# Performance work log

Measured on AMD Instinct MI355X. Metric: run time of the kernel, lower is better.

Reference implementation:

```python
import jax, jax.numpy as jnp
import numpy as np

B, T, DIM, S, DFF = 4, 2048, 2048, 4, 8192
SINKHORN_ITERS = 10


def setup_inputs() -> dict:
    key = jax.random.key(0)
    ks = jax.random.split(key, 12)

    def lin(k, fan_in, shape):
        bound = 1.0 / np.sqrt(fan_in)
        return jax.random.uniform(k, shape, jnp.float32, -bound, bound)

    return {
        "x": jax.random.normal(ks[0], (B, T, DIM), jnp.float32),
        # phi_* linears act on the S-times tiled vector of size S*DIM
        "phi_pre_w": lin(ks[1], S * DIM, (S, S * DIM)),
        "phi_pre_b": lin(ks[2], S * DIM, (S,)),
        "phi_post_w": lin(ks[3], S * DIM, (S, S * DIM)),
        "phi_post_b": lin(ks[4], S * DIM, (S,)),
        "phi_res_w": lin(ks[5], S * DIM, (S * S, S * DIM)),
        "phi_res_b": lin(ks[6], S * DIM, (S * S,)),
        "alpha_pre": jnp.ones((1,), jnp.float32),
        "alpha_post": jnp.ones((1,), jnp.float32),
        "alpha_res": jnp.ones((1,), jnp.float32),
        "b_pre": jnp.zeros((S,), jnp.float32),
        "b_post": jnp.zeros((S,), jnp.float32),
        "b_res": jnp.zeros((S, S), jnp.float32),
        # block = transformer MLP
        "W1": lin(ks[7], DIM, (DIM, DFF)),
        "b1": lin(ks[8], DIM, (DFF,)),
        "W2": lin(ks[9], DFF, (DFF, DIM)),
        "b2": lin(ks[10], DFF, (DIM,)),
    }


def sinkhorn_knopp(logits):
    # logits: [B, T, S, S] -> doubly-stochastic via exp + alternating normalization
    M = jnp.exp(logits)
    for _ in range(SINKHORN_ITERS):
        M = M / jnp.sum(M, axis=-1, keepdims=True)  # rows
        M = M / jnp.sum(M, axis=-2, keepdims=True)  # cols
    return M


def reference(x, phi_pre_w, phi_pre_b, phi_post_w, phi_post_b, phi_res_w,
              phi_res_b, alpha_pre, alpha_post, alpha_res, b_pre, b_post,
              b_res, W1, b1, W2, b2):
    bs, seq, d = x.shape
    s = b_pre.shape[0]
    eps = jnp.asarray(jnp.finfo(x.dtype).eps, x.dtype)
    # x_l = x expanded over S identical streams; x_vec = tile(x, S).
    # RMS over the tiled S*d vector == RMS over d (streams are copies).
    x_n = x * jax.lax.rsqrt(jnp.mean(x * x, axis=-1, keepdims=True) + eps)
    # Linear on the tiled vector == sum of the S weight blocks applied to x_n.
    Wp = phi_pre_w.reshape(s, s, d).sum(axis=1)        # [S, d]
    Wq = phi_post_w.reshape(s, s, d).sum(axis=1)       # [S, d]
    Wr = phi_res_w.reshape(s * s, s, d).sum(axis=1)    # [S*S, d]
    h_pre_t = alpha_pre * (jnp.einsum('btd,sd->bts', x_n, Wp) + phi_pre_b) + b_pre
    h_post_t = alpha_post * (jnp.einsum('btd,sd->bts', x_n, Wq) + phi_post_b) + b_post
    h_res_t = alpha_res * (jnp.einsum('btd,kd->btk', x_n, Wr) + phi_res_b)
    h_res_t = h_res_t.reshape(bs, seq, s, s) + b_res
    h_pre = jax.nn.sigmoid(h_pre_t)                    # [B,T,S]
    h_post = 2.0 * jax.nn.sigmoid(h_post_t)            # [B,T,S]
    h_res = sinkhorn_knopp(h_res_t)                    # [B,T,S,S]
    # block_input = sum_j x_l[:,:,j] * h_pre[...,j] ; streams identical -> x * sum_j h_pre
    block_input = x * jnp.sum(h_pre, axis=-1, keepdims=True)
    # block: MLP with exact (erf) GELU, matching torch default
    h = jax.nn.gelu(jnp.einsum('btd,df->btf', block_input, W1) + b1, approximate=False)
    block_out = jnp.einsum('btf,fd->btd', h, W2) + b2
    # out = sum_i [ (h_res @ x_l)_i + h_post_i * block_out ]
    #     = x * sum_{ij} h_res[ij] + block_out * sum_i h_post_i
    res_mix = jnp.sum(h_res, axis=(-2, -1))[..., None]         # [B,T,1]
    post_mix = jnp.sum(h_post, axis=-1, keepdims=True)          # [B,T,1]
    return x * res_mix + block_out * post_mix
```

## Files before the change

kernel.cpp:

```cpp
#include <hip/hip_runtime.h>
#include <hip/hip_bf16.h>
#include <cstdint>
#include <cstddef>

#define DIM   2048
#define DFF   8192
#define NROWS 8192
#define NFOLD 24

typedef float f32x4 __attribute__((ext_vector_type(4)));
typedef __bf16 bf16x8 __attribute__((ext_vector_type(8)));

__device__ __forceinline__ float sigmoidf_(float v) { return 1.0f / (1.0f + expf(-v)); }

__device__ __forceinline__ unsigned short f2bf(float v) {
    union { __hip_bfloat16 h; unsigned short u; } cv;
    cv.h = __float2bfloat16(v);
    return cv.u;
}

__device__ __forceinline__ void async_copy16(const void* g, void* l) {
    __builtin_amdgcn_global_load_lds((const __attribute__((address_space(1))) void*)g,
                                     (__attribute__((address_space(3))) void*)l, 16, 0, 0);
}

__device__ __forceinline__ void wg_barrier() {
    asm volatile("" ::: "memory");
    __builtin_amdgcn_s_barrier();
    asm volatile("" ::: "memory");
}

#define VM(n) asm volatile("s_waitcnt vmcnt(" #n ")" ::: "memory")
#define LGKM0 asm volatile("s_waitcnt lgkmcnt(0)" ::: "memory")

__global__ __launch_bounds__(256) void fold_kernel(const float* __restrict__ pre_w,
                                                   const float* __restrict__ post_w,
                                                   const float* __restrict__ res_w,
                                                   float* __restrict__ Wfold) {
    int idx = blockIdx.x * 256 + threadIdx.x;
    if (idx >= NFOLD * DIM) return;
    int r = idx >> 11;
    int d = idx & (DIM - 1);
    const float* src;
    if (r < 4)      src = pre_w  + (size_t)r * (4 * DIM);
    else if (r < 8) src = post_w + (size_t)(r - 4) * (4 * DIM);
    else            src = res_w  + (size_t)(r - 8) * (4 * DIM);
    Wfold[idx] = src[d] + src[DIM + d] + src[2 * DIM + d] + src[3 * DIM + d];
}

__global__ __launch_bounds__(256) void transpose_to_bf16(const float* __restrict__ in,
                                                         __hip_bfloat16* __restrict__ out,
                                                         int R, int C) {
    __shared__ float tile[32][33];
    int bx = blockIdx.x, by = blockIdx.y;
    int tx = threadIdx.x & 31, ty0 = threadIdx.x >> 5;
#pragma unroll
    for (int i = 0; i < 4; i++) {
        int ty = ty0 + i * 8;
        tile[ty][tx] = in[(size_t)(by * 32 + ty) * C + bx * 32 + tx];
    }
    __syncthreads();
#pragma unroll
    for (int i = 0; i < 4; i++) {
        int ty = ty0 + i * 8;
        out[(size_t)(bx * 32 + ty) * R + by * 32 + tx] = __float2bfloat16(tile[tx][ty]);
    }
}

__global__ __launch_bounds__(512) void gating_kernel(
    const float* __restrict__ x, const float* __restrict__ Wfold,
    const float* __restrict__ phi_pre_b, const float* __restrict__ phi_post_b,
    const float* __restrict__ phi_res_b,
    const float* __restrict__ alpha_pre, const float* __restrict__ alpha_post,
    const float* __restrict__ alpha_res,
    const float* __restrict__ b_pre, const float* __restrict__ b_post,
    const float* __restrict__ b_res,
    __hip_bfloat16* __restrict__ Abuf,
    float* __restrict__ g_res_arr, float* __restrict__ g_post_arr) {
    const int tid = threadIdx.x;
    const int lane = tid & 63, wave = tid >> 6;
    const int row = blockIdx.x * 8 + wave;

    const float4* x4 = (const float4*)x + (size_t)row * 512;
    const float4* w4 = (const float4*)Wfold;

    float4 xv[8];
#pragma unroll
    for (int j = 0; j < 8; j++) xv[j] = x4[j * 64 + lane];

    float p[25];
    p[24] = 0.f;
#pragma unroll
    for (int j = 0; j < 8; j++)
        p[24] += xv[j].x * xv[j].x + xv[j].y * xv[j].y + xv[j].z * xv[j].z + xv[j].w * xv[j].w;

    for (int r = 0; r < NFOLD; r++) {
        float acc = 0.f;
#pragma unroll
        for (int j = 0; j < 8; j++) {
            float4 wv = w4[r * 512 + j * 64 + lane];
            acc += xv[j].x * wv.x + xv[j].y * wv.y + xv[j].z * wv.z + xv[j].w * wv.w;
        }
        p[r] = acc;
    }

#pragma unroll
    for (int r = 0; r < 25; r++) {
        float v = p[r];
#pragma unroll
        for (int off = 1; off < 64; off <<= 1) v += __shfl_xor(v, off, 64);
        p[r] = v;
    }

    const float rms = rsqrtf(p[24] / (float)DIM + 1.1920928955078125e-07f);
    const float ap = alpha_pre[0], aq = alpha_post[0], ar = alpha_res[0];
    float gpre = 0.f, gpost = 0.f;
#pragma unroll
    for (int s = 0; s < 4; s++) {
        gpre  += sigmoidf_(ap * (rms * p[s]     + phi_pre_b[s])  + b_pre[s]);
        gpost += 2.0f * sigmoidf_(aq * (rms * p[4 + s] + phi_post_b[s]) + b_post[s]);
    }
    float Mm[4][4];
#pragma unroll
    for (int i = 0; i < 4; i++)
#pragma unroll
        for (int j = 0; j < 4; j++) {
            int k = i * 4 + j;
            Mm[i][j] = expf(ar * (rms * p[8 + k] + phi_res_b[k]) + b_res[k]);
        }
    for (int it = 0; it < 10; ++it) {
#pragma unroll
        for (int i = 0; i < 4; i++) {
            float rs = 1.0f / (Mm[i][0] + Mm[i][1] + Mm[i][2] + Mm[i][3]);
#pragma unroll
            for (int j = 0; j < 4; j++) Mm[i][j] *= rs;
        }
#pragma unroll
        for (int j = 0; j < 4; j++) {
            float cs = 1.0f / (Mm[0][j] + Mm[1][j] + Mm[2][j] + Mm[3][j]);
#pragma unroll
            for (int i = 0; i < 4; i++) Mm[i][j] *= cs;
        }
    }
    float gres = 0.f;
#pragma unroll
    for (int i = 0; i < 4; i++)
#pragma unroll
        for (int j = 0; j < 4; j++) gres += Mm[i][j];

    __hip_bfloat16* arow = Abuf + (size_t)row * DIM;
#pragma unroll
    for (int j = 0; j < 8; j++) {
        ushort4 u;
        u.x = f2bf(xv[j].x * gpre); u.y = f2bf(xv[j].y * gpre);
        u.z = f2bf(xv[j].z * gpre); u.w = f2bf(xv[j].w * gpre);
        *reinterpret_cast<ushort4*>(arow + (j * 64 + lane) * 4) = u;
    }
    if (lane == 0) {
        g_res_arr[row]  = gres;
        g_post_arr[row] = gpost;
    }
}

#define RD_A(DST, REG)                                                            \
    _Pragma("unroll") for (int m = 0; m < 4; ++m) {                               \
        DST[m][0] = *(const bf16x8*)((REG) + baseA + m * 2048 + cb0);             \
        DST[m][1] = *(const bf16x8*)((REG) + baseA + m * 2048 + cb1);             \
    }
#define RD_B(DST, REG)                                                            \
    _Pragma("unroll") for (int n = 0; n < 2; ++n) {                               \
        DST[n][0] = *(const bf16x8*)((REG) + baseB + n * 2048 + cb0);             \
        DST[n][1] = *(const bf16x8*)((REG) + baseB + n * 2048 + cb1);             \
    }

#define MQ(AF, BF, MO, NO)                                                        \
    __builtin_amdgcn_s_setprio(1);                                                \
    _Pragma("unroll") for (int m = 0; m < 4; ++m)                                 \
    _Pragma("unroll") for (int n = 0; n < 2; ++n) {                               \
        acc[(MO) + m][(NO) + n] = __builtin_amdgcn_mfma_f32_16x16x32_bf16(        \
            AF[m][0], BF[n][0], acc[(MO) + m][(NO) + n], 0, 0, 0);                \
        acc[(MO) + m][(NO) + n] = __builtin_amdgcn_mfma_f32_16x16x32_bf16(        \
            AF[m][1], BF[n][1], acc[(MO) + m][(NO) + n], 0, 0, 0);                \
    }                                                                             \
    __builtin_amdgcn_s_setprio(0);

#define STG_A(t_, h_)                                                             \
    if ((t_) < nk) {                                                              \
        char* l_ = ldsA + (((t_) & 1) * 32768) + (h_) * 16384 + wave * 1024;      \
        async_copy16(Ab + aOff[0][h_] + (size_t)(t_) * 128, l_);                  \
        async_copy16(Ab + aOff[1][h_] + (size_t)(t_) * 128, l_ + 8192);           \
    }
#define STG_B(t_, h_)                                                             \
    if ((t_) < nk) {                                                              \
        char* l_ = ldsB + (((t_) & 1) * 32768) + (h_) * 16384 + wave * 1024;      \
        async_copy16(Bb + bOff[0][h_] + (size_t)(t_) * 128, l_);                  \
        async_copy16(Bb + bOff[1][h_] + (size_t)(t_) * 128, l_ + 8192);           \
    }

template <int MODE, int NB>
__global__ __launch_bounds__(512, 2) void gemm256(
    const __hip_bfloat16* __restrict__ A, const __hip_bfloat16* __restrict__ Bt,
    int M, int N, int K, const float* __restrict__ bias,
    __hip_bfloat16* __restrict__ outh, float* __restrict__ outf,
    const float* __restrict__ x, const float* __restrict__ g_res,
    const float* __restrict__ g_post) {
    __shared__ __align__(16) char ldsA[65536];
    __shared__ __align__(16) char ldsB[65536];

    const int wg = blockIdx.x;
    const int xcd = wg & 7;
    const int i = wg >> 3;
    const int nt = xcd * NB + (i % NB);
    const int mt = i / NB;
    const int m0 = mt * 256;
    const int n0 = nt * 256;

    const int tid = threadIdx.x;
    const int lane = tid & 63;
    const int wave = tid >> 6;
    const int wr = wave >> 2;
    const int wc = wave & 3;
    const int q = lane >> 4;
    const int rr = lane & 7;

    const uint32_t cb0 = (uint32_t)((q ^ rr) << 4);
    const uint32_t cb1 = (uint32_t)(((4 + q) ^ rr) << 4);
    const uint32_t baseA = (uint32_t)((wr * 64 + (lane & 15)) * 128);
    const uint32_t baseB = (uint32_t)((wc * 32 + (lane & 15)) * 128);

    const uint32_t scb = (uint32_t)((((lane & 7) ^ ((lane >> 3) & 7))) << 4);
    const int lr = lane >> 3;
    const size_t K2 = (size_t)K * 2;
    size_t aOff[2][2], bOff[2][2];
#pragma unroll
    for (int ii = 0; ii < 2; ++ii)
#pragma unroll
        for (int h = 0; h < 2; ++h) {
            int gA = m0 + wave * 8 + lr + ii * 128 + h * 64;
            int gB = n0 + ((wave >> 2) + 2 * ii) * 64 + h * 32 + (wave & 3) * 8 + lr;
            aOff[ii][h] = (size_t)gA * K2 + scb;
            bOff[ii][h] = (size_t)gB * K2 + scb;
        }
    const char* Ab = (const char*)A;
    const char* Bb = (const char*)Bt;

    f32x4 acc[8][4];
#pragma unroll
    for (int m = 0; m < 8; ++m)
#pragma unroll
        for (int n = 0; n < 4; ++n) acc[m][n] = (f32x4){0.f, 0.f, 0.f, 0.f};

    const int nk = K / 64;

    STG_A(0, 0); STG_B(0, 0); STG_A(0, 1); STG_B(0, 1);
    STG_A(1, 0); STG_B(1, 0); STG_A(1, 1); STG_B(1, 1);
    VM(8);
    wg_barrier();

    bf16x8 a0[4][2], a1[4][2];
    bf16x8 b0[2][2], b1[2][2];
    RD_A(a0, ldsA)
    RD_B(b0, ldsB)
    LGKM0;
    wg_barrier();

    for (int kt = 0; kt < nk; ++kt) {
        const int c = kt & 1;
        const int cn = c ^ 1;
        const char* Ac = ldsA + c * 32768;
        const char* Bc = ldsB + c * 32768;
        const char* An = ldsA + cn * 32768;
        const char* Bn = ldsB + cn * 32768;
        const bool steady = (kt < nk - 2);
        RD_B(b1, Bc + 16384)
        STG_A(kt + 2, 0)
        MQ(a0, b0, 0, 0)
        LGKM0;
        if (steady) { VM(12); } else { VM(0); }
        wg_barrier();
        RD_A(a1, Ac + 16384)
        STG_B(kt + 2, 0)
        MQ(a0, b1, 0, 2)
        LGKM0;
        if (steady) { VM(10); } else { VM(0); }
        wg_barrier();
        if (kt + 1 < nk) { RD_A(a0, An) }
        STG_A(kt + 2, 1)
        MQ(a1, b0, 4, 0)
        LGKM0;
        if (steady) { VM(10); } else { VM(0); }
        wg_barrier();
        if (kt + 1 < nk) { RD_B(b0, Bn) }
        STG_B(kt + 2, 1)
        MQ(a1, b1, 4, 2)
        LGKM0;
        if (steady) { VM(8); } else { VM(0); }
        wg_barrier();
    }

#pragma unroll
    for (int mi = 0; mi < 8; ++mi) {
#pragma unroll
        for (int ni = 0; ni < 4; ++ni) {
            const int col = n0 + wc * 64 + (ni >> 1) * 32 + (ni & 1) * 16 + (lane & 15);
            const float bc = bias[col];
#pragma unroll
            for (int j = 0; j < 4; ++j) {
                const int row = m0 + wr * 128 + (mi >> 2) * 64 + (mi & 3) * 16 + q * 4 + j;
                float v = acc[mi][ni][j] + bc;
                if (MODE == 1) {
                    float u = 1.5957691216057308f * (v + 0.044715f * v * v * v);
                    float s = 1.0f / (1.0f + __expf(-u));
                    outh[(size_t)row * N + col] = __float2bfloat16(v * s);
                } else {
                    outf[(size_t)row * N + col] =
                        x[(size_t)row * N + col] * g_res[row] + v * g_post[row];
                }
            }
        }
    }
}

extern "C" void kernel_launch(void* const* d_in, const int* in_sizes, int n_in,
                              void* d_out, int out_size, void* d_ws, size_t ws_size,
                              hipStream_t stream) {
    const float* x          = (const float*)d_in[0];
    const float* phi_pre_w  = (const float*)d_in[1];
    const float* phi_pre_b  = (const float*)d_in[2];
    const float* phi_post_w = (const float*)d_in[3];
    const float* phi_post_b = (const float*)d_in[4];
    const float* phi_res_w  = (const float*)d_in[5];
    const float* phi_res_b  = (const float*)d_in[6];
    const float* alpha_pre  = (const float*)d_in[7];
    const float* alpha_post = (const float*)d_in[8];
    const float* alpha_res  = (const float*)d_in[9];
    const float* b_pre      = (const float*)d_in[10];
    const float* b_post     = (const float*)d_in[11];
    const float* b_res      = (const float*)d_in[12];
    const float* W1         = (const float*)d_in[13];
    const float* b1         = (const float*)d_in[14];
    const float* W2         = (const float*)d_in[15];
    const float* b2         = (const float*)d_in[16];
    float* out = (float*)d_out;

    char* ws = (char*)d_ws;
    __hip_bfloat16* W1T  = (__hip_bfloat16*)ws;
    __hip_bfloat16* W2T  = W1T + (size_t)DFF * DIM;
    __hip_bfloat16* Abuf = W2T + (size_t)DIM * DFF;
    __hip_bfloat16* Hbuf = Abuf + (size_t)NROWS * DIM;
    float* Wfold = (float*)(Hbuf + (size_t)NROWS * DFF);
    float* gres  = Wfold + NFOLD * DIM;
    float* gpost = gres + NROWS;

    fold_kernel<<<(NFOLD * DIM + 255) / 256, 256, 0, stream>>>(phi_pre_w, phi_post_w,
                                                               phi_res_w, Wfold);
    transpose_to_bf16<<<dim3(DFF / 32, DIM / 32), 256, 0, stream>>>(W1, W1T, DIM, DFF);
    transpose_to_bf16<<<dim3(DIM / 32, DFF / 32), 256, 0, stream>>>(W2, W2T, DFF, DIM);
    gating_kernel<<<NROWS / 8, 512, 0, stream>>>(x, Wfold, phi_pre_b, phi_post_b, phi_res_b,
                                                 alpha_pre, alpha_post, alpha_res,
                                                 b_pre, b_post, b_res, Abuf, gres, gpost);
    gemm256<1, 4><<<1024, 512, 0, stream>>>(
        Abuf, W1T, NROWS, DFF, DIM, b1, Hbuf, nullptr, nullptr, nullptr, nullptr);
    gemm256<2, 1><<<256, 512, 0, stream>>>(
        Hbuf, W2T, NROWS, DIM, DFF, b2, nullptr, out, x, gres, gpost);
}
```

Before: 690.3 us.

## Restructure GEMM main loop pipeline with 8-barrier schedule and sched barriers

```diff
diff --git a/kernel.cpp b/kernel.cpp
--- a/kernel.cpp
+++ b/kernel.cpp
@@ -30,8 +30,10 @@
     asm volatile("" ::: "memory");
 }
 
-#define VM(n) asm volatile("s_waitcnt vmcnt(" #n ")" ::: "memory")
-#define LGKM0 asm volatile("s_waitcnt lgkmcnt(0)" ::: "memory")
+#define VM(n)  asm volatile("s_waitcnt vmcnt(" #n ")" ::: "memory")
+#define LGKM0  asm volatile("s_waitcnt lgkmcnt(0)" ::: "memory")
+#define LGKM8  asm volatile("s_waitcnt lgkmcnt(8)" ::: "memory")
+#define SCHED0 __builtin_amdgcn_sched_barrier(0)
 
 __global__ __launch_bounds__(256) void fold_kernel(const float* __restrict__ pre_w,
                                                    const float* __restrict__ post_w,
@@ -252,49 +254,42 @@
 
     const int nk = K / 64;
 
-    STG_A(0, 0); STG_B(0, 0); STG_A(0, 1); STG_B(0, 1);
-    STG_A(1, 0); STG_B(1, 0); STG_A(1, 1); STG_B(1, 1);
-    VM(8);
+    STG_A(0, 0); STG_B(0, 0); STG_B(0, 1); STG_A(0, 1);
+    STG_A(1, 0); STG_B(1, 0); STG_A(1, 1);
+    VM(6);
     wg_barrier();
 
     bf16x8 a0[4][2], a1[4][2];
     bf16x8 b0[2][2], b1[2][2];
-    RD_A(a0, ldsA)
-    RD_B(b0, ldsB)
-    LGKM0;
-    wg_barrier();
 
     for (int kt = 0; kt < nk; ++kt) {
         const int c = kt & 1;
-        const int cn = c ^ 1;
         const char* Ac = ldsA + c * 32768;
         const char* Bc = ldsB + c * 32768;
-        const char* An = ldsA + cn * 32768;
-        const char* Bn = ldsB + cn * 32768;
-        const bool steady = (kt < nk - 2);
+        RD_A(a0, Ac)
+        RD_B(b0, Bc)
+        STG_B(kt + 1, 1)
+        LGKM8;
+        wg_barrier();
+        LGKM0; SCHED0;
+        MQ(a0, b0, 0, 0)
+        wg_barrier();
         RD_B(b1, Bc + 16384)
         STG_A(kt + 2, 0)
-        MQ(a0, b0, 0, 0)
-        LGKM0;
-        if (steady) { VM(12); } else { VM(0); }
+        wg_barrier();
+        LGKM0; SCHED0;
+        MQ(a0, b1, 0, 2)
         wg_barrier();
         RD_A(a1, Ac + 16384)
         STG_B(kt + 2, 0)
-        MQ(a0, b1, 0, 2)
-        LGKM0;
-        if (steady) { VM(10); } else { VM(0); }
-        wg_barrier();
-        if (kt + 1 < nk) { RD_A(a0, An) }
+        wg_barrier();
+        LGKM0; SCHED0;
+        MQ(a1, b0, 4, 0)
+        wg_barrier();
         STG_A(kt + 2, 1)
-        MQ(a1, b0, 4, 0)
-        LGKM0;
-        if (steady) { VM(10); } else { VM(0); }
-        wg_barrier();
-        if (kt + 1 < nk) { RD_B(b0, Bn) }
-        STG_B(kt + 2, 1)
+        if (kt + 2 < nk) { VM(6); } else { VM(0); }
+        wg_barrier();
         MQ(a1, b1, 4, 2)
-        LGKM0;
-        if (steady) { VM(8); } else { VM(0); }
         wg_barrier();
     }
 
```

After: 651.1 us. -5.7%, faster.
